# Performance work log

Measured on AMD Instinct MI355X. Metric: run time of the kernel, lower is better.

Reference implementation:

```python
import jax, jax.numpy as jnp
import numpy as np

N = 100000   # nodes
D = 128      # feature dim
E = 1600000  # edges (avg degree 16)
BN_EPS = 1e-5


def setup_inputs() -> dict:
    key = jax.random.key(0)
    ks = jax.random.split(key, 8)
    x = jax.random.normal(ks[0], (N, D), dtype=jnp.float32)
    edge_index = jax.random.randint(ks[1], (2, E), 0, N, dtype=jnp.int64)
    W = jax.random.normal(ks[2], (D, D), dtype=jnp.float32) * 0.05   # GCNConv linear weight
    b = jax.random.normal(ks[3], (D,), dtype=jnp.float32) * 0.05     # GCNConv bias
    gamma = jax.random.uniform(ks[4], (D,), dtype=jnp.float32) + 0.5 # BN weight
    beta = jax.random.normal(ks[5], (D,), dtype=jnp.float32) * 0.1   # BN bias
    running_mean = jax.random.normal(ks[6], (D,), dtype=jnp.float32) * 0.1
    running_var = jax.random.uniform(ks[7], (D,), dtype=jnp.float32) + 0.5
    return {"x": x, "edge_index": edge_index, "W": W, "b": b,
            "gamma": gamma, "beta": beta,
            "running_mean": running_mean, "running_var": running_var}


def reference(x, edge_index, W, b, gamma, beta, running_mean, running_var):
    # --- GCNConv (default: add self-loops, symmetric normalization) ---
    h = x @ W                                        # [N, D]
    loops = jnp.arange(N, dtype=edge_index.dtype)
    src = jnp.concatenate([edge_index[0], loops])    # [E+N]
    dst = jnp.concatenate([edge_index[1], loops])    # [E+N]
    deg = jax.ops.segment_sum(jnp.ones_like(dst, dtype=h.dtype), dst, num_segments=N)
    dinv = jax.lax.rsqrt(jnp.maximum(deg, 1.0))      # deg >= 1 due to self-loops
    norm = dinv[src] * dinv[dst]                     # [E+N]
    agg = jax.ops.segment_sum(h[src] * norm[:, None], dst, num_segments=N)  # [N, D]
    agg = agg + b
    # --- BatchNorm1d (inference: running stats) ---
    bn = (agg - running_mean) * jax.lax.rsqrt(running_var + BN_EPS) * gamma + beta
    # --- ReLU + residual (dropout is identity in eval) ---
    return jax.nn.relu(bn) + x
```

## Files before the change

kernel.cpp:

```cpp
#include <hip/hip_runtime.h>

#define D 128
#define BN_EPS 1e-5f
#define NBUCK 512
#define BSHIFT 8
#define BNODES 256

using short8 = __attribute__((ext_vector_type(8))) short;
using floatx4 = __attribute__((ext_vector_type(4))) float;

__device__ inline unsigned short f2bf(float f) {
    unsigned u = __float_as_uint(f);
    u += 0x7fff + ((u >> 16) & 1);
    return (unsigned short)(u >> 16);
}
__device__ inline float bf2f(unsigned short s) {
    return __uint_as_float(((unsigned)s) << 16);
}

__global__ void wt_kernel(const float* __restrict__ W, const float* __restrict__ b,
                          const float* __restrict__ gamma, const float* __restrict__ beta,
                          const float* __restrict__ mean, const float* __restrict__ var,
                          unsigned short* __restrict__ Wt, float* __restrict__ scv,
                          float* __restrict__ pov, int* __restrict__ bucketTot,
                          int* __restrict__ resCnt) {
    int t = blockIdx.x * blockDim.x + threadIdx.x;
    int k = t >> 7, n = t & 127;
    Wt[(size_t)n * D + k] = f2bf(W[t]);
    if (t < D) {
        float sc = gamma[t] * rsqrtf(var[t] + BN_EPS);
        scv[t] = sc;
        pov[t] = (b[t] - mean[t]) * sc + beta[t];
    }
    if (t < NBUCK) {
        bucketTot[t] = 0;
        resCnt[t] = 0;
    }
}

__global__ __launch_bounds__(512) void pA_kernel(const int* __restrict__ dst,
                                                 int* __restrict__ bucketTot, int E) {
    __shared__ int lh[NBUCK];
    int tid = threadIdx.x;
    lh[tid] = 0;
    __syncthreads();
    for (int i = blockIdx.x * 512 + tid; i < E; i += gridDim.x * 512)
        atomicAdd(&lh[dst[i] >> BSHIFT], 1);
    __syncthreads();
    if (lh[tid]) atomicAdd(&bucketTot[tid], lh[tid]);
}

__global__ __launch_bounds__(512) void pB_kernel(const int* __restrict__ src,
                                                 const int* __restrict__ dst,
                                                 const int* __restrict__ bucketTot,
                                                 int* __restrict__ resCnt,
                                                 int2* __restrict__ pairs, int E) {
    __shared__ int sb[NBUCK];
    __shared__ int lh[NBUCK];
    __shared__ int lcur[NBUCK];
    int tid = threadIdx.x;
    sb[tid] = bucketTot[tid];
    lh[tid] = 0;
    __syncthreads();
    for (int d = 1; d < NBUCK; d <<= 1) {
        int v = (tid >= d) ? sb[tid - d] : 0;
        __syncthreads();
        sb[tid] += v;
        __syncthreads();
    }
    int chunk = (E + gridDim.x - 1) / gridDim.x;
    int base = blockIdx.x * chunk;
    int lim = min(chunk, E - base);
    if (lim <= 0) return;
    for (int i = tid; i < lim; i += 512) atomicAdd(&lh[dst[base + i] >> BSHIFT], 1);
    __syncthreads();
    int c = lh[tid];
    lcur[tid] = c ? (sb[tid] - bucketTot[tid]) + atomicAdd(&resCnt[tid], c) : 0;
    __syncthreads();
    for (int i = tid; i < lim; i += 512) {
        int s = src[base + i], d2 = dst[base + i];
        int pos = atomicAdd(&lcur[d2 >> BSHIFT], 1);
        pairs[pos] = make_int2(s, d2);
    }
}

__global__ __launch_bounds__(512) void sort_kernel(const int2* __restrict__ pairs,
                                                   const int* __restrict__ bucketTot,
                                                   int* __restrict__ deg,
                                                   int* __restrict__ offs,
                                                   int* __restrict__ colidx, int N, int E) {
    __shared__ int sb[NBUCK];
    __shared__ int lh[BNODES];
    __shared__ int lcur[BNODES];
    int tid = threadIdx.x;
    int b = blockIdx.x;
    sb[tid] = bucketTot[tid];
    __syncthreads();
    for (int d = 1; d < NBUCK; d <<= 1) {
        int v = (tid >= d) ? sb[tid - d] : 0;
        __syncthreads();
        sb[tid] += v;
        __syncthreads();
    }
    int cnt = bucketTot[b];
    int base = sb[b] - cnt;
    if (tid < BNODES) lh[tid] = 0;
    __syncthreads();
    for (int i = tid; i < cnt; i += 512)
        atomicAdd(&lh[pairs[base + i].y & (BNODES - 1)], 1);
    __syncthreads();
    int orig = (tid < BNODES) ? lh[tid] : 0;
    for (int d = 1; d < BNODES; d <<= 1) {
        int v = (tid < BNODES && tid >= d) ? lh[tid - d] : 0;
        __syncthreads();
        if (tid < BNODES) lh[tid] += v;
        __syncthreads();
    }
    if (tid < BNODES) {
        int exc = lh[tid] - orig;
        int node = b * BNODES + tid;
        if (node < N) {
            deg[node] = orig;
            offs[node] = base + exc;
        }
        lcur[tid] = exc;
    }
    if (b == 0 && tid == 0) offs[N] = E;
    __syncthreads();
    for (int i = tid; i < cnt; i += 512) {
        int2 p = pairs[base + i];
        int pos = atomicAdd(&lcur[p.y & (BNODES - 1)], 1);
        colidx[base + pos] = p.x;
    }
}

__global__ void xs_kernel(const float* __restrict__ x, const int* __restrict__ deg,
                          float* __restrict__ dinv, unsigned short* __restrict__ xs,
                          int total4) {
    int i = blockIdx.x * blockDim.x + threadIdx.x;
    if (i >= total4) return;
    int node = i >> 5, q = i & 31;
    float dv = rsqrtf((float)(deg[node] + 1));
    if (q == 0) dinv[node] = dv;
    float4 f = ((const float4*)x)[i];
    ushort4 o;
    o.x = f2bf(dv * f.x); o.y = f2bf(dv * f.y);
    o.z = f2bf(dv * f.z); o.w = f2bf(dv * f.w);
    ((ushort4*)xs)[i] = o;
}

__global__ void deg_kernel(const int* __restrict__ dst, int* __restrict__ deg, int E) {
    int e = blockIdx.x * blockDim.x + threadIdx.x;
    if (e < E) atomicAdd(&deg[dst[e]], 1);
}

__global__ void dinv_kernel(const int* __restrict__ deg, float* __restrict__ dinv, int N) {
    int v = blockIdx.x * blockDim.x + threadIdx.x;
    if (v < N) dinv[v] = rsqrtf((float)(deg[v] + 1));
}

__global__ __launch_bounds__(256) void scan1_kernel(const int* __restrict__ deg,
                                                    int* __restrict__ bsum, int N) {
    __shared__ int s[256];
    int t = threadIdx.x;
    int v = blockIdx.x * 256 + t;
    s[t] = (v < N) ? deg[v] : 0;
    for (int st = 128; st > 0; st >>= 1) {
        __syncthreads();
        if (t < st) s[t] += s[t + st];
    }
    if (t == 0) bsum[blockIdx.x] = s[0];
}

__global__ __launch_bounds__(512) void scan2_kernel(int* __restrict__ bsum,
                                                    int* __restrict__ offs, int P, int N) {
    __shared__ int a[512];
    int t = threadIdx.x;
    int orig = (t < P) ? bsum[t] : 0;
    a[t] = orig;
    __syncthreads();
    for (int d = 1; d < 512; d <<= 1) {
        int tv = (t >= d) ? a[t - d] : 0;
        __syncthreads();
        a[t] += tv;
        __syncthreads();
    }
    if (t < P) bsum[t] = a[t] - orig;
    if (t == 0) offs[N] = a[511];
}

__global__ __launch_bounds__(256) void scan3_kernel(const int* __restrict__ deg,
                                                    const int* __restrict__ bsum,
                                                    int* __restrict__ offs,
                                                    int* __restrict__ cursor, int N) {
    __shared__ int a[256];
    int t = threadIdx.x;
    int v = blockIdx.x * 256 + t;
    int d = (v < N) ? deg[v] : 0;
    a[t] = d;
    __syncthreads();
    for (int st = 1; st < 256; st <<= 1) {
        int tv = (t >= st) ? a[t - st] : 0;
        __syncthreads();
        a[t] += tv;
        __syncthreads();
    }
    if (v < N) {
        int off = bsum[blockIdx.x] + a[t] - d;
        offs[v] = off;
        cursor[v] = off;
    }
}

__global__ void fill_kernel(const int* __restrict__ src, const int* __restrict__ dst,
                            int* __restrict__ cursor, int* __restrict__ colidx, int E) {
    int e = blockIdx.x * blockDim.x + threadIdx.x;
    if (e < E) {
        int d = dst[e];
        int pos = atomicAdd(&cursor[d], 1);
        colidx[pos] = src[e];
    }
}

__global__ __launch_bounds__(256) void agg_kernel(
    const float* __restrict__ x, const unsigned short* __restrict__ xs,
    const float* __restrict__ dinv, const int* __restrict__ offs,
    const int* __restrict__ colidx, float* __restrict__ outp,
    unsigned int* __restrict__ aggb, int N) {
    int wid = (blockIdx.x * blockDim.x + threadIdx.x) >> 6;
    if (wid >= N) return;
    int lane = threadIdx.x & 63;
    float dv = dinv[wid];
    float a0, a1;
    int p = offs[wid], pe = offs[wid + 1];
    if (xs) {
        const unsigned int* xs32 = (const unsigned int*)xs;
        unsigned int sv = xs32[(size_t)wid * 64 + lane];
        a0 = bf2f((unsigned short)sv);
        a1 = bf2f((unsigned short)(sv >> 16));
        for (; p + 16 <= pe; p += 16) {
            int u[16];
            unsigned int v[16];
#pragma unroll
            for (int j = 0; j < 16; ++j) u[j] = colidx[p + j];
#pragma unroll
            for (int j = 0; j < 16; ++j) v[j] = xs32[(size_t)u[j] * 64 + lane];
#pragma unroll
            for (int j = 0; j < 16; ++j) {
                a0 += bf2f((unsigned short)v[j]);
                a1 += bf2f((unsigned short)(v[j] >> 16));
            }
        }
        for (; p + 4 <= pe; p += 4) {
            int u[4];
            unsigned int v[4];
#pragma unroll
            for (int j = 0; j < 4; ++j) u[j] = colidx[p + j];
#pragma unroll
            for (int j = 0; j < 4; ++j) v[j] = xs32[(size_t)u[j] * 64 + lane];
#pragma unroll
            for (int j = 0; j < 4; ++j) {
                a0 += bf2f((unsigned short)v[j]);
                a1 += bf2f((unsigned short)(v[j] >> 16));
            }
        }
        for (; p < pe; ++p) {
            unsigned int v = xs32[(size_t)colidx[p] * 64 + lane];
            a0 += bf2f((unsigned short)v);
            a1 += bf2f((unsigned short)(v >> 16));
        }
        aggb[(size_t)wid * 64 + lane] =
            (unsigned int)f2bf(dv * a0) | ((unsigned int)f2bf(dv * a1) << 16);
    } else {
        const float2* x2 = (const float2*)x;
        float2 s = x2[(size_t)wid * 64 + lane];
        a0 = dv * s.x;
        a1 = dv * s.y;
        for (; p < pe; ++p) {
            int u = colidx[p];
            float du = dinv[u];
            float2 vv = x2[(size_t)u * 64 + lane];
            a0 += du * vv.x;
            a1 += du * vv.y;
        }
        float2 r;
        r.x = dv * a0;
        r.y = dv * a1;
        ((float2*)outp)[(size_t)wid * 64 + lane] = r;
    }
}

__global__ __launch_bounds__(256) void gemm_kernel(
    float* __restrict__ outp, const float* __restrict__ xg,
    const unsigned short* __restrict__ Wt, const unsigned short* __restrict__ aggb,
    const float* __restrict__ scv, const float* __restrict__ pov, int nTiles) {
    int wid = (blockIdx.x * blockDim.x + threadIdx.x) >> 6;
    if (wid >= nTiles) return;
    int lane = threadIdx.x & 63;
    int m = lane & 15, quad = lane >> 4;
    int row0 = wid * 16;

    short8 B[8][4];
#pragma unroll
    for (int cg = 0; cg < 8; ++cg)
#pragma unroll
        for (int ks = 0; ks < 4; ++ks)
            B[cg][ks] = *(const short8*)&Wt[(size_t)(cg * 16 + m) * D + ks * 32 + quad * 8];

    short8 A[4];
    if (aggb) {
        const unsigned short* arow = aggb + (size_t)(row0 + m) * D;
#pragma unroll
        for (int ks = 0; ks < 4; ++ks)
            A[ks] = *(const short8*)&arow[ks * 32 + quad * 8];
    } else {
        const float* arow = outp + (size_t)(row0 + m) * D;
#pragma unroll
        for (int ks = 0; ks < 4; ++ks) {
            float4 f0 = *(const float4*)(arow + ks * 32 + quad * 8);
            float4 f1 = *(const float4*)(arow + ks * 32 + quad * 8 + 4);
            short8 af;
            af[0] = (short)f2bf(f0.x); af[1] = (short)f2bf(f0.y);
            af[2] = (short)f2bf(f0.z); af[3] = (short)f2bf(f0.w);
            af[4] = (short)f2bf(f1.x); af[5] = (short)f2bf(f1.y);
            af[6] = (short)f2bf(f1.z); af[7] = (short)f2bf(f1.w);
            A[ks] = af;
        }
    }

#pragma unroll
    for (int cg = 0; cg < 8; ++cg) {
        floatx4 acc = {0.f, 0.f, 0.f, 0.f};
#pragma unroll
        for (int ks = 0; ks < 4; ++ks)
            acc = __builtin_amdgcn_mfma_f32_16x16x32_bf16(A[ks], B[cg][ks], acc, 0, 0, 0);
        int col = cg * 16 + m;
        float sc = scv[col], po = pov[col];
#pragma unroll
        for (int i = 0; i < 4; ++i) {
            int row = row0 + quad * 4 + i;
            float bn = acc[i] * sc + po;
            size_t idx = (size_t)row * D + col;
            outp[idx] = fmaxf(bn, 0.f) + xg[idx];
        }
    }
}

extern "C" void kernel_launch(void* const* d_in, const int* in_sizes, int n_in,
                              void* d_out, int out_size, void* d_ws, size_t ws_size,
                              hipStream_t stream) {
    const float* x = (const float*)d_in[0];
    const int* edge = (const int*)d_in[1];
    const float* Wm = (const float*)d_in[2];
    const float* b = (const float*)d_in[3];
    const float* gamma = (const float*)d_in[4];
    const float* beta = (const float*)d_in[5];
    const float* mean = (const float*)d_in[6];
    const float* var = (const float*)d_in[7];
    float* out = (float*)d_out;

    int N = in_sizes[0] / D;
    int E = in_sizes[1] / 2;
    const int* src = edge;
    const int* dst = edge + E;
    int P = (N + 255) / 256;

    char* w = (char*)d_ws;
    size_t cur = 0;
    auto take = [&](size_t bytes) -> void* {
        cur = (cur + 15) & ~(size_t)15;
        void* p = w + cur;
        cur += bytes;
        return p;
    };
    int* deg = (int*)take((size_t)N * 4);
    int* bucketTot = (int*)take(NBUCK * 4);
    int* resCnt = (int*)take(NBUCK * 4);
    float* dinv = (float*)take((size_t)N * 4);
    int* offs = (int*)take((size_t)(N + 1) * 4);
    int* cursor = (int*)take((size_t)N * 4);
    int* bsum = (int*)take((size_t)(P + 1) * 4);
    unsigned short* Wt = (unsigned short*)take((size_t)D * D * 2);
    float* scv = (float*)take(D * 4);
    float* pov = (float*)take(D * 4);
    int* colidx = (int*)take((size_t)E * 4);
    cur = (cur + 15) & ~(size_t)15;
    size_t fixedEnd = cur;

    size_t xsBytes = (size_t)N * D * 2;
    size_t zoneBytes = (xsBytes > (size_t)E * 8) ? xsBytes : (size_t)E * 8;
    bool fast = fixedEnd + xsBytes + zoneBytes <= ws_size;

    unsigned short* xs = nullptr;
    int2* pairs = nullptr;
    unsigned int* aggb = nullptr;
    if (fast) {
        xs = (unsigned short*)(w + fixedEnd);
        pairs = (int2*)(w + fixedEnd + xsBytes);
        aggb = (unsigned int*)(w + fixedEnd + xsBytes);
    }

    wt_kernel<<<(D * D) / 256, 256, 0, stream>>>(Wm, b, gamma, beta, mean, var, Wt, scv,
                                                 pov, bucketTot, resCnt);

    if (fast) {
        pA_kernel<<<1024, 512, 0, stream>>>(dst, bucketTot, E);
        pB_kernel<<<1024, 512, 0, stream>>>(src, dst, bucketTot, resCnt, pairs, E);
        sort_kernel<<<NBUCK, 512, 0, stream>>>(pairs, bucketTot, deg, offs, colidx, N, E);
        xs_kernel<<<(N * 32 + 255) / 256, 256, 0, stream>>>(x, deg, dinv, xs, N * 32);
    } else {
        hipMemsetAsync(deg, 0, sizeof(int) * N, stream);
        deg_kernel<<<(E + 255) / 256, 256, 0, stream>>>(dst, deg, E);
        dinv_kernel<<<(N + 255) / 256, 256, 0, stream>>>(deg, dinv, N);
        scan1_kernel<<<P, 256, 0, stream>>>(deg, bsum, N);
        scan2_kernel<<<1, 512, 0, stream>>>(bsum, offs, P, N);
        scan3_kernel<<<P, 256, 0, stream>>>(deg, bsum, offs, cursor, N);
        fill_kernel<<<(E + 255) / 256, 256, 0, stream>>>(src, dst, cursor, colidx, E);
    }
    agg_kernel<<<(N * 64 + 255) / 256, 256, 0, stream>>>(x, xs, dinv, offs, colidx, out, aggb, N);
    int nTiles = (N + 15) / 16;
    gemm_kernel<<<(nTiles * 64 + 255) / 256, 256, 0, stream>>>(
        out, x, Wt, (const unsigned short*)aggb, scv, pov, nTiles);
}
```

Before: 301.7 us.

## Fuse weight prep into histogram, xs scaling into sort, stage W in LDS

Folds the weight transpose/BN-constant kernel into the bucket-histogram kernel. Folds the dinv computation and bf16 scaling of x into the per-bucket sort kernel, reusing the degrees already held in shared memory. Bucket counters are now zeroed with a memset, which assumes resCnt sits right after bucketTot. The GEMM kernel stages the bf16 weight matrix in swizzled LDS instead of holding 128 VGPRs of B fragments per wave, which trades register pressure and occupancy for LDS reads and a block-level sync.

```diff
diff --git a/kernel.cpp b/kernel.cpp
--- a/kernel.cpp
+++ b/kernel.cpp
@@ -22,8 +22,7 @@
                           const float* __restrict__ gamma, const float* __restrict__ beta,
                           const float* __restrict__ mean, const float* __restrict__ var,
                           unsigned short* __restrict__ Wt, float* __restrict__ scv,
-                          float* __restrict__ pov, int* __restrict__ bucketTot,
-                          int* __restrict__ resCnt) {
+                          float* __restrict__ pov) {
     int t = blockIdx.x * blockDim.x + threadIdx.x;
     int k = t >> 7, n = t & 127;
     Wt[(size_t)n * D + k] = f2bf(W[t]);
@@ -32,20 +31,34 @@
         scv[t] = sc;
         pov[t] = (b[t] - mean[t]) * sc + beta[t];
     }
-    if (t < NBUCK) {
-        bucketTot[t] = 0;
-        resCnt[t] = 0;
-    }
-}
-
-__global__ __launch_bounds__(512) void pA_kernel(const int* __restrict__ dst,
-                                                 int* __restrict__ bucketTot, int E) {
+}
+
+__global__ __launch_bounds__(512) void pAwt_kernel(
+    const int* __restrict__ dst, int* __restrict__ bucketTot, int E,
+    const float* __restrict__ W, const float* __restrict__ b,
+    const float* __restrict__ gamma, const float* __restrict__ beta,
+    const float* __restrict__ mean, const float* __restrict__ var,
+    unsigned short* __restrict__ Wt, float* __restrict__ scv,
+    float* __restrict__ pov) {
     __shared__ int lh[NBUCK];
     int tid = threadIdx.x;
     lh[tid] = 0;
     __syncthreads();
     for (int i = blockIdx.x * 512 + tid; i < E; i += gridDim.x * 512)
         atomicAdd(&lh[dst[i] >> BSHIFT], 1);
+    if (blockIdx.x < 16) {
+        int t = blockIdx.x * 512 + tid;
+#pragma unroll
+        for (int h = 0; h < 2; ++h) {
+            int tt = t + h * 8192;
+            Wt[(size_t)(tt & 127) * D + (tt >> 7)] = f2bf(W[tt]);
+        }
+        if (blockIdx.x == 0 && tid < D) {
+            float sc = gamma[tid] * rsqrtf(var[tid] + BN_EPS);
+            scv[tid] = sc;
+            pov[tid] = (b[tid] - mean[tid]) * sc + beta[tid];
+        }
+    }
     __syncthreads();
     if (lh[tid]) atomicAdd(&bucketTot[tid], lh[tid]);
 }
@@ -84,14 +97,15 @@
     }
 }
 
-__global__ __launch_bounds__(512) void sort_kernel(const int2* __restrict__ pairs,
-                                                   const int* __restrict__ bucketTot,
-                                                   int* __restrict__ deg,
-                                                   int* __restrict__ offs,
-                                                   int* __restrict__ colidx, int N, int E) {
+__global__ __launch_bounds__(512) void sortxs_kernel(
+    const int2* __restrict__ pairs, const int* __restrict__ bucketTot,
+    const float* __restrict__ x, int* __restrict__ deg, int* __restrict__ offs,
+    int* __restrict__ colidx, float* __restrict__ dinv,
+    unsigned short* __restrict__ xs, int N, int E) {
     __shared__ int sb[NBUCK];
     __shared__ int lh[BNODES];
     __shared__ int lcur[BNODES];
+    __shared__ float sdv[BNODES];
     int tid = threadIdx.x;
     int b = blockIdx.x;
     sb[tid] = bucketTot[tid];
@@ -119,9 +133,12 @@
     if (tid < BNODES) {
         int exc = lh[tid] - orig;
         int node = b * BNODES + tid;
+        float dvv = rsqrtf((float)(orig + 1));
+        sdv[tid] = dvv;
         if (node < N) {
             deg[node] = orig;
             offs[node] = base + exc;
+            dinv[node] = dvv;
         }
         lcur[tid] = exc;
     }
@@ -132,21 +149,22 @@
         int pos = atomicAdd(&lcur[p.y & (BNODES - 1)], 1);
         colidx[base + pos] = p.x;
     }
-}
-
-__global__ void xs_kernel(const float* __restrict__ x, const int* __restrict__ deg,
-                          float* __restrict__ dinv, unsigned short* __restrict__ xs,
-                          int total4) {
-    int i = blockIdx.x * blockDim.x + threadIdx.x;
-    if (i >= total4) return;
-    int node = i >> 5, q = i & 31;
-    float dv = rsqrtf((float)(deg[node] + 1));
-    if (q == 0) dinv[node] = dv;
-    float4 f = ((const float4*)x)[i];
-    ushort4 o;
-    o.x = f2bf(dv * f.x); o.y = f2bf(dv * f.y);
-    o.z = f2bf(dv * f.z); o.w = f2bf(dv * f.w);
-    ((ushort4*)xs)[i] = o;
+    int nb = min(BNODES, N - b * BNODES);
+    if (nb > 0) {
+        const float4* x4 = (const float4*)x;
+        ushort4* xs4 = (ushort4*)xs;
+        int tot = nb * 32;
+        for (int c = tid; c < tot; c += 512) {
+            int nl = c >> 5, q = c & 31;
+            int node = b * BNODES + nl;
+            float dvv = sdv[nl];
+            float4 f = x4[(size_t)node * 32 + q];
+            ushort4 o;
+            o.x = f2bf(dvv * f.x); o.y = f2bf(dvv * f.y);
+            o.z = f2bf(dvv * f.z); o.w = f2bf(dvv * f.w);
+            xs4[(size_t)node * 32 + q] = o;
+        }
+    }
 }
 
 __global__ void deg_kernel(const int* __restrict__ dst, int* __restrict__ deg, int E) {
@@ -294,18 +312,22 @@
     float* __restrict__ outp, const float* __restrict__ xg,
     const unsigned short* __restrict__ Wt, const unsigned short* __restrict__ aggb,
     const float* __restrict__ scv, const float* __restrict__ pov, int nTiles) {
-    int wid = (blockIdx.x * blockDim.x + threadIdx.x) >> 6;
+    __shared__ uint4 sW4[2048];
+    int tid = threadIdx.x;
+    const uint4* W4 = (const uint4*)Wt;
+#pragma unroll
+    for (int i = 0; i < 8; ++i) {
+        int q = tid + i * 256;
+        int row = q >> 4, c4 = q & 15;
+        sW4[row * 16 + (c4 ^ (row & 7))] = W4[q];
+    }
+    __syncthreads();
+
+    int wid = (blockIdx.x * blockDim.x + tid) >> 6;
     if (wid >= nTiles) return;
-    int lane = threadIdx.x & 63;
+    int lane = tid & 63;
     int m = lane & 15, quad = lane >> 4;
     int row0 = wid * 16;
-
-    short8 B[8][4];
-#pragma unroll
-    for (int cg = 0; cg < 8; ++cg)
-#pragma unroll
-        for (int ks = 0; ks < 4; ++ks)
-            B[cg][ks] = *(const short8*)&Wt[(size_t)(cg * 16 + m) * D + ks * 32 + quad * 8];
 
     short8 A[4];
     if (aggb) {
@@ -330,10 +352,13 @@
 
 #pragma unroll
     for (int cg = 0; cg < 8; ++cg) {
+        int brow = cg * 16 + m;
         floatx4 acc = {0.f, 0.f, 0.f, 0.f};
 #pragma unroll
-        for (int ks = 0; ks < 4; ++ks)
-            acc = __builtin_amdgcn_mfma_f32_16x16x32_bf16(A[ks], B[cg][ks], acc, 0, 0, 0);
+        for (int ks = 0; ks < 4; ++ks) {
+            short8 Bf = *(const short8*)&sW4[brow * 16 + ((ks * 4 + quad) ^ (m & 7))];
+            acc = __builtin_amdgcn_mfma_f32_16x16x32_bf16(A[ks], Bf, acc, 0, 0, 0);
+        }
         int col = cg * 16 + m;
         float sc = scv[col], po = pov[col];
 #pragma unroll
@@ -400,15 +425,16 @@
         aggb = (unsigned int*)(w + fixedEnd + xsBytes);
     }
 
-    wt_kernel<<<(D * D) / 256, 256, 0, stream>>>(Wm, b, gamma, beta, mean, var, Wt, scv,
-                                                 pov, bucketTot, resCnt);
-
     if (fast) {
-        pA_kernel<<<1024, 512, 0, stream>>>(dst, bucketTot, E);
+        hipMemsetAsync(bucketTot, 0, (size_t)NBUCK * 8, stream);
+        pAwt_kernel<<<1024, 512, 0, stream>>>(dst, bucketTot, E, Wm, b, gamma, beta,
+                                              mean, var, Wt, scv, pov);
         pB_kernel<<<1024, 512, 0, stream>>>(src, dst, bucketTot, resCnt, pairs, E);
-        sort_kernel<<<NBUCK, 512, 0, stream>>>(pairs, bucketTot, deg, offs, colidx, N, E);
-        xs_kernel<<<(N * 32 + 255) / 256, 256, 0, stream>>>(x, deg, dinv, xs, N * 32);
+        sortxs_kernel<<<NBUCK, 512, 0, stream>>>(pairs, bucketTot, x, deg, offs, colidx,
+                                                 dinv, xs, N, E);
     } else {
+        wt_kernel<<<(D * D) / 256, 256, 0, stream>>>(Wm, b, gamma, beta, mean, var, Wt,
+                                                     scv, pov);
         hipMemsetAsync(deg, 0, sizeof(int) * N, stream);
         deg_kernel<<<(E + 255) / 256, 256, 0, stream>>>(dst, deg, E);
         dinv_kernel<<<(N + 255) / 256, 256, 0, stream>>>(deg, dinv, N);
@@ -417,7 +443,8 @@
         scan3_kernel<<<P, 256, 0, stream>>>(deg, bsum, offs, cursor, N);
         fill_kernel<<<(E + 255) / 256, 256, 0, stream>>>(src, dst, cursor, colidx, E);
     }
-    agg_kernel<<<(N * 64 + 255) / 256, 256, 0, stream>>>(x, xs, dinv, offs, colidx, out, aggb, N);
+    agg_kernel<<<(N * 64 + 255) / 256, 256, 0, stream>>>(x, xs, dinv, offs, colidx, out,
+                                                         aggb, N);
     int nTiles = (N + 15) / 16;
     gemm_kernel<<<(nTiles * 64 + 255) / 256, 256, 0, stream>>>(
         out, x, Wt, (const unsigned short*)aggb, scv, pov, nTiles);
```

Result: faster. 286.7 us (-5.0%).
